# Kernel optimization log

Measured on AMD Instinct MI355X. Metric: run time of the kernel, lower is better.

## Reference

```python
import jax, jax.numpy as jnp
import numpy as np

B = 4; E_PER = 100_000; E = B * E_PER
N_NODES = 50_000; N_REL = 500; D = 64; D_LG = 256
K_PER_VI = 20; S_VI = E // K_PER_VI          # 20000 sorted vi segments
S_VJ_PER = 5_000; S_VJ = B * S_VJ_PER        # 20000 unsorted vj segments
N_MEM = 131_072
INTERACT = ((0, 3), (0, 2, 3), (0, 4), (0, 2, 4), (1, 3), (1, 2, 3), (1, 4), (1, 2, 4))


def _build_edges():
    rng = np.random.default_rng(0)
    idx_vi = np.repeat(np.arange(S_VI), K_PER_VI)          # sorted segment ids
    gpb = S_VI // B
    eg = idx_vi // gpb                                     # sorted by eg_idx too
    vi = rng.integers(0, N_NODES, S_VI)[idx_vi]
    idx_vj = np.empty(E, dtype=np.int64)
    for b in range(B):
        loc = np.concatenate([np.arange(S_VJ_PER), rng.integers(0, S_VJ_PER, E_PER - S_VJ_PER)])
        rng.shuffle(loc)
        idx_vj[b * E_PER:(b + 1) * E_PER] = b * S_VJ_PER + loc  # every group non-empty
    vj = rng.integers(0, N_NODES, S_VJ)[idx_vj]            # consistent (eg, vj) per group
    rel = rng.integers(0, N_REL, E)
    e2vi = rng.integers(0, N_MEM, E)
    e2vj = rng.integers(0, N_MEM, E)
    return np.stack([eg, vi, vj, rel, idx_vi, idx_vj, e2vi, e2vj], axis=1).astype(np.int32)


def setup_inputs() -> dict:
    key = jax.random.key(0)
    ks = jax.random.split(key, 10)
    return {
        "node_attention": jax.random.uniform(ks[0], (B, N_NODES), jnp.float32),
        "scanned_edges": jnp.asarray(_build_edges()),
        "edges_y": jax.random.uniform(ks[1], (E,), jnp.float32),
        "hidden_uncon": jax.random.normal(ks[2], (1, N_NODES, D_LG), jnp.float32),
        "hidden_con": jax.random.normal(ks[3], (N_MEM, D), jnp.float32),
        "Wc": jax.random.normal(ks[4], (D, D), jnp.float32) / np.sqrt(D).astype(np.float32),
        "bc": jnp.zeros((D,), jnp.float32),
        "Wu": jax.random.normal(ks[5], (D_LG, D), jnp.float32) / np.sqrt(D_LG).astype(np.float32),
        "bu": jnp.zeros((D,), jnp.float32),
        "rel_table": jax.random.normal(ks[6], (N_REL, D), jnp.float32) * 0.05,
        "ws": jax.random.normal(ks[7], (len(INTERACT), D), jnp.float32) / np.sqrt(float(len(INTERACT))).astype(np.float32) if False else jax.random.normal(ks[7], (len(INTERACT), D), jnp.float32) * (1.0 / np.sqrt(len(INTERACT)).astype(np.float32)),
        "fb": jnp.zeros((D,), jnp.float32),
        "out_w": jax.random.normal(ks[8], (D,), jnp.float32),
        "out_b": jnp.zeros((D,), jnp.float32),
        "n_vi_segments": S_VI,
        "n_vj_segments": S_VJ,
    }


def reference(node_attention, scanned_edges, edges_y, hidden_uncon, hidden_con,
              Wc, bc, Wu, bu, rel_table, ws, fb, out_w, out_b,
              n_vi_segments, n_vj_segments):
    eg, vi, vj, rel = (scanned_edges[:, i] for i in range(4))
    idx_vi, idx_vj, e2vi, e2vj = (scanned_edges[:, i] for i in range(4, 8))
    # projections (proj_con / proj_uncon, tanh Dense)
    hc = jnp.tanh(hidden_con @ Wc + bc)          # [N_MEM, D]
    hu = jnp.tanh(hidden_uncon @ Wu + bu)[0]     # [n_nodes, D]; batch_size==1 path of Node2Edge
    # Node2Edge gathers
    feats = (hc[e2vi], hu[vi], rel_table[rel], hc[e2vj], hu[vj])  # each [E, D]
    # F layer: weighted sum of elementwise interaction products
    out = fb
    for k, idxs in enumerate(INTERACT):
        x = feats[idxs[0]]
        for i in idxs[1:]:
            x = x * feats[i]
        out = out + x * ws[k]
    out = jax.nn.relu(out) * out_w + out_b
    logits = jnp.sum(out, axis=1)                # [E]
    # NeighborSoftmax at 'vi' (sorted segment softmax)
    m = jax.ops.segment_max(logits, idx_vi, num_segments=n_vi_segments)
    ex = jnp.exp(logits - m[idx_vi])
    den = jax.ops.segment_sum(ex, idx_vi, num_segments=n_vi_segments)
    transition = ex / den[idx_vi]
    # attention flow: gather source attention, weight, aggregate at vj
    trans_att = transition * node_attention[eg, vi] * edges_y
    aggr = jax.ops.segment_sum(trans_att, idx_vj, num_segments=n_vj_segments)
    b_g = jax.ops.segment_max(eg, idx_vj, num_segments=n_vj_segments)
    vj_g = jax.ops.segment_max(vj, idx_vj, num_segments=n_vj_segments)
    new_node_attention = jnp.zeros_like(node_attention).at[b_g, vj_g].add(aggr)
    return new_node_attention
```

## Files before the change

### kernel.cpp

```cpp
#include <hip/hip_runtime.h>
#include <hip/hip_bf16.h>
#include <hip/hip_fp16.h>

#define D 64
#define KPER 20

typedef __attribute__((ext_vector_type(8))) short short8;
typedef __attribute__((ext_vector_type(4))) float floatx4;

__device__ __forceinline__ unsigned short f2bfu(float x) {
    __hip_bfloat16 h = __float2bfloat16(x);
    return *reinterpret_cast<unsigned short*>(&h);
}
__device__ __forceinline__ unsigned short f2hu(float x) {
    __half h = __float2half(x);
    return *reinterpret_cast<unsigned short*>(&h);
}
union UH2 { unsigned u; __half2 h; };
__device__ __forceinline__ __half2 u2h2(unsigned u) { UH2 x; x.u = u; return x.h; }

__device__ __forceinline__ __half2 pk_max(__half2 a, __half2 b) {
    __half2 r;
    asm("v_pk_max_f16 %0, %1, %2" : "=v"(r) : "v"(a), "v"(b));
    return r;
}

__device__ __forceinline__ float fast_tanh(float x) {
    float xc = fminf(fmaxf(x, -15.f), 15.f);
    float e = __expf(2.f * xc);
    return 1.f - 2.f * __builtin_amdgcn_rcpf(1.f + e);
}

template<int CTRL>
__device__ __forceinline__ float dpp_add(float x) {
    int t = __builtin_amdgcn_update_dpp(0, __float_as_int(x), CTRL, 0xf, 0xf, true);
    return x + __int_as_float(t);
}
template<int CTRL>
__device__ __forceinline__ float dpp_max(float x) {
    int xi = __float_as_int(x);
    int t = __builtin_amdgcn_update_dpp(xi, xi, CTRL, 0xf, 0xf, false);
    return fmaxf(x, __int_as_float(t));
}
__device__ __forceinline__ float wave_sum_b(float x) {
    x = dpp_add<0x111>(x); x = dpp_add<0x112>(x);
    x = dpp_add<0x114>(x); x = dpp_add<0x118>(x);
    x = dpp_add<0x142>(x); x = dpp_add<0x143>(x);
    return __int_as_float(__builtin_amdgcn_readlane(__float_as_int(x), 63));
}
__device__ __forceinline__ float wave_max_b(float x) {
    x = dpp_max<0x111>(x); x = dpp_max<0x112>(x);
    x = dpp_max<0x114>(x); x = dpp_max<0x118>(x);
    x = dpp_max<0x142>(x); x = dpp_max<0x143>(x);
    return __int_as_float(__builtin_amdgcn_readlane(__float_as_int(x), 63));
}
__device__ __forceinline__ float row16_sum(float x) {
    x = dpp_add<0x111>(x); x = dpp_add<0x112>(x);
    x = dpp_add<0x114>(x); x = dpp_add<0x118>(x);
    return x;
}

__global__ __launch_bounds__(256) void prep(
        const float* __restrict__ Wc, const float* __restrict__ Wu,
        const float* __restrict__ relf, const float* __restrict__ wsf,
        const float* __restrict__ fbf,
        unsigned short* __restrict__ Wcp, unsigned short* __restrict__ Wup,
        unsigned short* __restrict__ relb, unsigned short* __restrict__ wsh,
        unsigned short* __restrict__ fbh, float* __restrict__ outz,
        int nout, int nrel) {
    int tid = blockIdx.x * 256 + threadIdx.x;
    int nth = gridDim.x * 256;
    for (int i = tid; i < 4 * 2 * 64 * 8; i += nth) {
        int j = i & 7, lane = (i >> 3) & 63, f = i >> 9;
        int ct = f >> 1, kt = f & 1;
        int m = lane & 15, quad = lane >> 4;
        Wcp[i] = f2bfu(Wc[(kt * 32 + quad * 8 + j) * 64 + ct * 16 + m]);
    }
    for (int i = tid; i < 4 * 8 * 64 * 8; i += nth) {
        int j = i & 7, lane = (i >> 3) & 63, f = i >> 9;
        int ct = f >> 3, kt = f & 7;
        int m = lane & 15, quad = lane >> 4;
        Wup[i] = f2bfu(Wu[(kt * 32 + quad * 8 + j) * 64 + ct * 16 + m]);
    }
    for (int i = tid; i < nrel; i += nth) relb[i] = f2hu(relf[i]);
    for (int i = tid; i < 8 * D; i += nth) wsh[i] = f2hu(wsf[i]);
    for (int i = tid; i < D; i += nth) fbh[i] = f2hu(fbf[i]);
    for (int i = tid; i < nout; i += nth) outz[i] = 0.0f;
}

__device__ __forceinline__ void proj64_pair(const float* __restrict__ h,
        const unsigned short* __restrict__ Wp, const float* __restrict__ b,
        unsigned short* __restrict__ out, int rt0) {
    constexpr int K = 64, KT = 2, CTN = 4;
    int lane = threadIdx.x & 63;
    int m = lane & 15, quad = lane >> 4;
    short8 bfr[CTN][KT];
    #pragma unroll
    for (int ct = 0; ct < CTN; ++ct)
        #pragma unroll
        for (int kt = 0; kt < KT; ++kt)
            bfr[ct][kt] = *(const short8*)(Wp + (((ct * 2 + kt) * 64 + lane) << 3));
    float bv[CTN];
    #pragma unroll
    for (int ct = 0; ct < CTN; ++ct) bv[ct] = b[ct * 16 + m];
    int rt1 = rt0 + 1;
    const float* hrow0 = h + (size_t)(rt0 * 16 + m) * K + quad * 8;
    const float* hrow1 = h + (size_t)(rt1 * 16 + m) * K + quad * 8;
    floatx4 a0[KT][2], a1[KT][2];
    #pragma unroll
    for (int kt = 0; kt < KT; ++kt) {
        a0[kt][0] = *(const floatx4*)(hrow0 + kt * 32);
        a0[kt][1] = *(const floatx4*)(hrow0 + kt * 32 + 4);
        a1[kt][0] = *(const floatx4*)(hrow1 + kt * 32);
        a1[kt][1] = *(const floatx4*)(hrow1 + kt * 32 + 4);
    }
    #pragma unroll
    for (int t = 0; t < 2; ++t) {
        floatx4 (*ar)[2] = t ? a1 : a0;
        int rt = t ? rt1 : rt0;
        floatx4 acc[CTN];
        #pragma unroll
        for (int ct = 0; ct < CTN; ++ct) acc[ct] = floatx4{0.f, 0.f, 0.f, 0.f};
        #pragma unroll
        for (int kt = 0; kt < KT; ++kt) {
            short8 af;
            #pragma unroll
            for (int j = 0; j < 4; ++j) {
                af[j]     = (short)f2bfu(ar[kt][0][j]);
                af[j + 4] = (short)f2bfu(ar[kt][1][j]);
            }
            #pragma unroll
            for (int ct = 0; ct < CTN; ++ct)
                acc[ct] = __builtin_amdgcn_mfma_f32_16x16x32_bf16(af, bfr[ct][kt], acc[ct], 0, 0, 0);
        }
        #pragma unroll
        for (int ct = 0; ct < CTN; ++ct) {
            int col = ct * 16 + m;
            #pragma unroll
            for (int reg = 0; reg < 4; ++reg) {
                int row = rt * 16 + quad * 4 + reg;
                out[(size_t)row * 64 + col] = f2hu(fast_tanh(acc[ct][reg] + bv[ct]));
            }
        }
    }
}

__device__ __forceinline__ void proj256_body(const float* __restrict__ h,
        const unsigned short* __restrict__ Wp, const float* __restrict__ b,
        unsigned short* __restrict__ out, int ct0, int rt0, int rtstride, int ntiles) {
    constexpr int K = 256, KT = 8, CTN = 2;
    int lane = threadIdx.x & 63;
    int m = lane & 15, quad = lane >> 4;
    short8 bfr[CTN][KT];
    #pragma unroll
    for (int ct = 0; ct < CTN; ++ct)
        #pragma unroll
        for (int kt = 0; kt < KT; ++kt)
            bfr[ct][kt] = *(const short8*)(Wp + ((((ct0 + ct) * 8 + kt) * 64 + lane) << 3));
    float bv[CTN];
    #pragma unroll
    for (int ct = 0; ct < CTN; ++ct) bv[ct] = b[(ct0 + ct) * 16 + m];
    for (int rt = rt0; rt < ntiles; rt += rtstride) {
        floatx4 acc[CTN];
        #pragma unroll
        for (int ct = 0; ct < CTN; ++ct) acc[ct] = floatx4{0.f, 0.f, 0.f, 0.f};
        const float* hrow = h + (size_t)(rt * 16 + m) * K + quad * 8;
        #pragma unroll
        for (int kt = 0; kt < KT; ++kt) {
            floatx4 v0 = *(const floatx4*)(hrow + kt * 32);
            floatx4 v1 = *(const floatx4*)(hrow + kt * 32 + 4);
            short8 af;
            #pragma unroll
            for (int j = 0; j < 4; ++j) {
                af[j]     = (short)f2bfu(v0[j]);
                af[j + 4] = (short)f2bfu(v1[j]);
            }
            #pragma unroll
            for (int ct = 0; ct < CTN; ++ct)
                acc[ct] = __builtin_amdgcn_mfma_f32_16x16x32_bf16(af, bfr[ct][kt], acc[ct], 0, 0, 0);
        }
        #pragma unroll
        for (int ct = 0; ct < CTN; ++ct) {
            int col = (ct0 + ct) * 16 + m;
            #pragma unroll
            for (int reg = 0; reg < 4; ++reg) {
                int row = rt * 16 + quad * 4 + reg;
                out[(size_t)row * 64 + col] = f2hu(fast_tanh(acc[ct][reg] + bv[ct]));
            }
        }
    }
}

__global__ __launch_bounds__(256) void proj_fused(
        const float* __restrict__ hcon, const unsigned short* __restrict__ Wcp,
        const float* __restrict__ bc,
        const float* __restrict__ hun, const unsigned short* __restrict__ Wup,
        const float* __restrict__ bu,
        unsigned short* __restrict__ hc, unsigned short* __restrict__ hu,
        int t64, int t256, int g64, int g256) {
    int bid = blockIdx.x;
    int w = threadIdx.x >> 6;
    if (bid < g256) {
        int wid = bid * 4 + w;
        int half = wid & 1;
        proj256_body(hun, Wup, bu, hu, half * 2, wid >> 1, g256 * 2, t256);
    } else {
        int wid = (bid - g256) * 4 + w;
        proj64_pair(hcon, Wcp, bc, hc, wid * 2);
    }
}

__device__ __forceinline__ float seg_myl(
        const uint2* __restrict__ G0, const uint2* __restrict__ G2,
        const uint2* __restrict__ G3, const uint2* __restrict__ G4,
        uint2 F1u, const uint2* __restrict__ wku, uint2 fbu, floatx4 owv,
        int lane, int l2, __half2 z2) {
    __half2 f1[2]  = { u2h2(F1u.x), u2h2(F1u.y) };
    __half2 fb2[2] = { u2h2(fbu.x), u2h2(fbu.y) };
    float myl = -INFINITY;
    #pragma unroll
    for (int i = 0; i < 5; ++i) {
        float acc = 0.f;
        #pragma unroll
        for (int p = 0; p < 2; ++p) {
            __half2 F0 = u2h2(p ? G0[i].y : G0[i].x);
            __half2 F2 = u2h2(p ? G2[i].y : G2[i].x);
            __half2 F3 = u2h2(p ? G3[i].y : G3[i].x);
            __half2 F4 = u2h2(p ? G4[i].y : G4[i].x);
            __half2 w0 = u2h2(p ? wku[0].y : wku[0].x);
            __half2 w1 = u2h2(p ? wku[1].y : wku[1].x);
            __half2 w2 = u2h2(p ? wku[2].y : wku[2].x);
            __half2 w3 = u2h2(p ? wku[3].y : wku[3].x);
            __half2 w4 = u2h2(p ? wku[4].y : wku[4].x);
            __half2 w5 = u2h2(p ? wku[5].y : wku[5].x);
            __half2 w6 = u2h2(p ? wku[6].y : wku[6].x);
            __half2 w7 = u2h2(p ? wku[7].y : wku[7].x);
            __half2 t1 = __hfma2(F2, w1, w0);
            __half2 t2 = __hfma2(F2, w5, w4);
            __half2 t3 = __hfma2(F2, w3, w2);
            __half2 t4 = __hfma2(F2, w7, w6);
            __half2 uu = __hfma2(F0, t1, __hmul2(f1[p], t2));
            __half2 vv = __hfma2(F0, t3, __hmul2(f1[p], t4));
            __half2 od = __hfma2(F3, uu, __hfma2(F4, vv, fb2[p]));
            __half2 r  = pk_max(od, z2);
            float2 rf  = __half22float2(r);
            acc = fmaf(rf.x, owv[2 * p], fmaf(rf.y, owv[2 * p + 1], acc));
        }
        float rs = row16_sum(acc);
        float tot = __shfl(rs, ((lane & 3) << 4) + 15);
        myl = (l2 == i) ? tot : myl;
    }
    return myl;
}

__global__ __launch_bounds__(256) void edge_kernel(
        const float* __restrict__ natt, const int* __restrict__ edges,
        const float* __restrict__ ey, const unsigned short* __restrict__ hc,
        const unsigned short* __restrict__ hu, const unsigned short* __restrict__ relt,
        const unsigned short* __restrict__ wsh, const unsigned short* __restrict__ fbh,
        const float* __restrict__ outw, float* __restrict__ out, int N) {
    int lane = threadIdx.x & 63;
    int g = lane >> 4, sub = lane & 15;
    int l2 = lane >> 2;
    int wid = blockIdx.x * 4 + (threadIdx.x >> 6);
    long baseA = (long)(wid * 2) * KPER;
    long baseB = baseA + KPER;
    const int* ebA = edges + baseA * 8;
    const int* ebB = edges + baseB * 8;

    int2 h0A = *(const int2*)ebA;
    int2 h0B = *(const int2*)ebB;
    const int* egpA = ebA + g * 8;
    const int* egpB = ebB + g * 8;
    int2 m23A[5], m67A[5], m23B[5], m67B[5];
    #pragma unroll
    for (int i = 0; i < 5; ++i) {
        m23A[i] = *(const int2*)(egpA + i * 32 + 2);
        m67A[i] = *(const int2*)(egpA + i * 32 + 6);
        m23B[i] = *(const int2*)(egpB + i * 32 + 2);
        m67B[i] = *(const int2*)(egpB + i * 32 + 6);
    }
    int myvjA = 0, myvjB = 0; float eyA = 0.f, eyB = 0.f;
    if (lane < KPER) {
        myvjA = ebA[lane * 8 + 2];
        myvjB = ebB[lane * 8 + 2];
        eyA = ey[baseA + lane];
        eyB = ey[baseB + lane];
    }
    int egA = __builtin_amdgcn_readfirstlane(h0A.x);
    int viA = __builtin_amdgcn_readfirstlane(h0A.y);
    int egB = __builtin_amdgcn_readfirstlane(h0B.x);
    int viB = __builtin_amdgcn_readfirstlane(h0B.y);

    uint2 GA0[5], GA2[5], GA3[5], GA4[5];
    #pragma unroll
    for (int i = 0; i < 5; ++i) {
        GA0[i] = *(const uint2*)(hc   + (size_t)m67A[i].x * D + sub * 4);
        GA2[i] = *(const uint2*)(relt + (size_t)m23A[i].y * D + sub * 4);
        GA3[i] = *(const uint2*)(hc   + (size_t)m67A[i].y * D + sub * 4);
        GA4[i] = *(const uint2*)(hu   + (size_t)m23A[i].x * D + sub * 4);
    }
    uint2 F1A = *(const uint2*)(hu + (size_t)viA * D + sub * 4);
    uint2 GB0[5], GB2[5], GB3[5], GB4[5];
    #pragma unroll
    for (int i = 0; i < 5; ++i) {
        GB0[i] = *(const uint2*)(hc   + (size_t)m67B[i].x * D + sub * 4);
        GB2[i] = *(const uint2*)(relt + (size_t)m23B[i].y * D + sub * 4);
        GB3[i] = *(const uint2*)(hc   + (size_t)m67B[i].y * D + sub * 4);
        GB4[i] = *(const uint2*)(hu   + (size_t)m23B[i].x * D + sub * 4);
    }
    uint2 F1B = *(const uint2*)(hu + (size_t)viB * D + sub * 4);
    float naA = natt[(size_t)egA * N + viA];
    float naB = natt[(size_t)egB * N + viB];

    uint2 wku[8];
    #pragma unroll
    for (int k = 0; k < 8; ++k) wku[k] = *(const uint2*)(wsh + k * D + sub * 4);
    uint2 fbu = *(const uint2*)(fbh + sub * 4);
    floatx4 owv = *(const floatx4*)(outw + sub * 4);
    __half2 z2 = __float2half2_rn(0.f);

    float mylA = seg_myl(GA0, GA2, GA3, GA4, F1A, wku, fbu, owv, lane, l2, z2);
    float mxA = wave_max_b(mylA);
    float exA = __expf(mylA - mxA);
    float denA = wave_sum_b(exA);
    if (lane < KPER) {
        float t = (exA / denA) * naA * eyA;
        atomicAdd(out + (size_t)egA * N + myvjA, t);
    }
    float mylB = seg_myl(GB0, GB2, GB3, GB4, F1B, wku, fbu, owv, lane, l2, z2);
    float mxB = wave_max_b(mylB);
    float exB = __expf(mylB - mxB);
    float denB = wave_sum_b(exB);
    if (lane < KPER) {
        float t = (exB / denB) * naB * eyB;
        atomicAdd(out + (size_t)egB * N + myvjB, t);
    }
}

extern "C" void kernel_launch(void* const* d_in, const int* in_sizes, int n_in,
                              void* d_out, int out_size, void* d_ws, size_t ws_size,
                              hipStream_t stream) {
    const float* natt = (const float*)d_in[0];
    const int*   edges = (const int*)d_in[1];
    const float* ey   = (const float*)d_in[2];
    const float* hun  = (const float*)d_in[3];
    const float* hcon = (const float*)d_in[4];
    const float* Wc   = (const float*)d_in[5];
    const float* bc   = (const float*)d_in[6];
    const float* Wu   = (const float*)d_in[7];
    const float* bu   = (const float*)d_in[8];
    const float* relt = (const float*)d_in[9];
    const float* wsm  = (const float*)d_in[10];
    const float* fb   = (const float*)d_in[11];
    const float* outw = (const float*)d_in[12];
    float* out = (float*)d_out;

    int E    = in_sizes[2];
    int S    = E / KPER;
    int nmem = in_sizes[4] / D;
    int N    = in_sizes[3] / 256;
    int nrel = in_sizes[9];

    int t64  = nmem / 16;
    int t256 = N / 16;
    int g64  = t64 / 8;
    int g256 = 800;

    unsigned short* hc  = (unsigned short*)d_ws;
    unsigned short* hu  = hc + (size_t)nmem * D;
    unsigned short* rb  = hu + (size_t)N * D;
    unsigned short* Wcp = rb + nrel;
    unsigned short* Wup = Wcp + 4096;
    unsigned short* wsh = Wup + 16384;
    unsigned short* fbh = wsh + 8 * D;

    prep<<<64, 256, 0, stream>>>(Wc, Wu, relt, wsm, fb, Wcp, Wup, rb, wsh, fbh,
                                 out, out_size, nrel);
    proj_fused<<<g256 + g64, 256, 0, stream>>>(hcon, Wcp, bc, hun, Wup, bu,
                                               hc, hu, t64, t256, g64, g256);
    edge_kernel<<<S / 8, 256, 0, stream>>>(natt, edges, ey, hc, hu, rb,
                                           wsh, fbh, outw, out, N);
}
```

Baseline: 198.1 us.

## Split edge kernel into logits kernel and segment softmax-scatter kernel

Replaces the fused per-segment edge kernel, which had each wave hold two full 20-edge segments of gathered features in registers, with two kernels. The first computes per-edge logits with 16 lanes per edge in a simple loop and writes them to a workspace buffer. The second does the segment softmax and atomic scatter per segment. This is meant to cut register pressure and raise occupancy for the gather-heavy part. The cost is an extra launch plus a write and re-read of the logits array.

Result: slower. 225.7 us (+14.0%).

```diff
diff --git a/kernel.cpp b/kernel.cpp
--- a/kernel.cpp
+++ b/kernel.cpp
@@ -210,108 +210,48 @@
     }
 }
 
-__device__ __forceinline__ float seg_myl(
-        const uint2* __restrict__ G0, const uint2* __restrict__ G2,
-        const uint2* __restrict__ G3, const uint2* __restrict__ G4,
-        uint2 F1u, const uint2* __restrict__ wku, uint2 fbu, floatx4 owv,
-        int lane, int l2, __half2 z2) {
-    __half2 f1[2]  = { u2h2(F1u.x), u2h2(F1u.y) };
-    __half2 fb2[2] = { u2h2(fbu.x), u2h2(fbu.y) };
-    float myl = -INFINITY;
-    #pragma unroll
-    for (int i = 0; i < 5; ++i) {
-        float acc = 0.f;
-        #pragma unroll
-        for (int p = 0; p < 2; ++p) {
-            __half2 F0 = u2h2(p ? G0[i].y : G0[i].x);
-            __half2 F2 = u2h2(p ? G2[i].y : G2[i].x);
-            __half2 F3 = u2h2(p ? G3[i].y : G3[i].x);
-            __half2 F4 = u2h2(p ? G4[i].y : G4[i].x);
-            __half2 w0 = u2h2(p ? wku[0].y : wku[0].x);
-            __half2 w1 = u2h2(p ? wku[1].y : wku[1].x);
-            __half2 w2 = u2h2(p ? wku[2].y : wku[2].x);
-            __half2 w3 = u2h2(p ? wku[3].y : wku[3].x);
-            __half2 w4 = u2h2(p ? wku[4].y : wku[4].x);
-            __half2 w5 = u2h2(p ? wku[5].y : wku[5].x);
-            __half2 w6 = u2h2(p ? wku[6].y : wku[6].x);
-            __half2 w7 = u2h2(p ? wku[7].y : wku[7].x);
-            __half2 t1 = __hfma2(F2, w1, w0);
-            __half2 t2 = __hfma2(F2, w5, w4);
-            __half2 t3 = __hfma2(F2, w3, w2);
-            __half2 t4 = __hfma2(F2, w7, w6);
-            __half2 uu = __hfma2(F0, t1, __hmul2(f1[p], t2));
-            __half2 vv = __hfma2(F0, t3, __hmul2(f1[p], t4));
-            __half2 od = __hfma2(F3, uu, __hfma2(F4, vv, fb2[p]));
-            __half2 r  = pk_max(od, z2);
-            float2 rf  = __half22float2(r);
-            acc = fmaf(rf.x, owv[2 * p], fmaf(rf.y, owv[2 * p + 1], acc));
-        }
-        float rs = row16_sum(acc);
-        float tot = __shfl(rs, ((lane & 3) << 4) + 15);
-        myl = (l2 == i) ? tot : myl;
-    }
-    return myl;
-}
-
-__global__ __launch_bounds__(256) void edge_kernel(
-        const float* __restrict__ natt, const int* __restrict__ edges,
-        const float* __restrict__ ey, const unsigned short* __restrict__ hc,
+__device__ __forceinline__ float edge_acc(
+        uint2 G0, uint2 G2, uint2 G3, uint2 G4, uint2 F1u,
+        const uint2* __restrict__ wku, uint2 fbu, floatx4 owv, __half2 z2) {
+    float acc = 0.f;
+    #pragma unroll
+    for (int p = 0; p < 2; ++p) {
+        __half2 F0 = u2h2(p ? G0.y : G0.x);
+        __half2 F2 = u2h2(p ? G2.y : G2.x);
+        __half2 F3 = u2h2(p ? G3.y : G3.x);
+        __half2 F4 = u2h2(p ? G4.y : G4.x);
+        __half2 f1 = u2h2(p ? F1u.y : F1u.x);
+        __half2 fb2 = u2h2(p ? fbu.y : fbu.x);
+        __half2 w0 = u2h2(p ? wku[0].y : wku[0].x);
+        __half2 w1 = u2h2(p ? wku[1].y : wku[1].x);
+        __half2 w2 = u2h2(p ? wku[2].y : wku[2].x);
+        __half2 w3 = u2h2(p ? wku[3].y : wku[3].x);
+        __half2 w4 = u2h2(p ? wku[4].y : wku[4].x);
+        __half2 w5 = u2h2(p ? wku[5].y : wku[5].x);
+        __half2 w6 = u2h2(p ? wku[6].y : wku[6].x);
+        __half2 w7 = u2h2(p ? wku[7].y : wku[7].x);
+        __half2 t1 = __hfma2(F2, w1, w0);
+        __half2 t2 = __hfma2(F2, w5, w4);
+        __half2 t3 = __hfma2(F2, w3, w2);
+        __half2 t4 = __hfma2(F2, w7, w6);
+        __half2 uu = __hfma2(F0, t1, __hmul2(f1, t2));
+        __half2 vv = __hfma2(F0, t3, __hmul2(f1, t4));
+        __half2 od = __hfma2(F3, uu, __hfma2(F4, vv, fb2));
+        __half2 r  = pk_max(od, z2);
+        float2 rf  = __half22float2(r);
+        acc = fmaf(rf.x, owv[2 * p], fmaf(rf.y, owv[2 * p + 1], acc));
+    }
+    return acc;
+}
+
+__global__ __launch_bounds__(256) void logits_kernel(
+        const int* __restrict__ edges, const unsigned short* __restrict__ hc,
         const unsigned short* __restrict__ hu, const unsigned short* __restrict__ relt,
         const unsigned short* __restrict__ wsh, const unsigned short* __restrict__ fbh,
-        const float* __restrict__ outw, float* __restrict__ out, int N) {
-    int lane = threadIdx.x & 63;
-    int g = lane >> 4, sub = lane & 15;
-    int l2 = lane >> 2;
-    int wid = blockIdx.x * 4 + (threadIdx.x >> 6);
-    long baseA = (long)(wid * 2) * KPER;
-    long baseB = baseA + KPER;
-    const int* ebA = edges + baseA * 8;
-    const int* ebB = edges + baseB * 8;
-
-    int2 h0A = *(const int2*)ebA;
-    int2 h0B = *(const int2*)ebB;
-    const int* egpA = ebA + g * 8;
-    const int* egpB = ebB + g * 8;
-    int2 m23A[5], m67A[5], m23B[5], m67B[5];
-    #pragma unroll
-    for (int i = 0; i < 5; ++i) {
-        m23A[i] = *(const int2*)(egpA + i * 32 + 2);
-        m67A[i] = *(const int2*)(egpA + i * 32 + 6);
-        m23B[i] = *(const int2*)(egpB + i * 32 + 2);
-        m67B[i] = *(const int2*)(egpB + i * 32 + 6);
-    }
-    int myvjA = 0, myvjB = 0; float eyA = 0.f, eyB = 0.f;
-    if (lane < KPER) {
-        myvjA = ebA[lane * 8 + 2];
-        myvjB = ebB[lane * 8 + 2];
-        eyA = ey[baseA + lane];
-        eyB = ey[baseB + lane];
-    }
-    int egA = __builtin_amdgcn_readfirstlane(h0A.x);
-    int viA = __builtin_amdgcn_readfirstlane(h0A.y);
-    int egB = __builtin_amdgcn_readfirstlane(h0B.x);
-    int viB = __builtin_amdgcn_readfirstlane(h0B.y);
-
-    uint2 GA0[5], GA2[5], GA3[5], GA4[5];
-    #pragma unroll
-    for (int i = 0; i < 5; ++i) {
-        GA0[i] = *(const uint2*)(hc   + (size_t)m67A[i].x * D + sub * 4);
-        GA2[i] = *(const uint2*)(relt + (size_t)m23A[i].y * D + sub * 4);
-        GA3[i] = *(const uint2*)(hc   + (size_t)m67A[i].y * D + sub * 4);
-        GA4[i] = *(const uint2*)(hu   + (size_t)m23A[i].x * D + sub * 4);
-    }
-    uint2 F1A = *(const uint2*)(hu + (size_t)viA * D + sub * 4);
-    uint2 GB0[5], GB2[5], GB3[5], GB4[5];
-    #pragma unroll
-    for (int i = 0; i < 5; ++i) {
-        GB0[i] = *(const uint2*)(hc   + (size_t)m67B[i].x * D + sub * 4);
-        GB2[i] = *(const uint2*)(relt + (size_t)m23B[i].y * D + sub * 4);
-        GB3[i] = *(const uint2*)(hc   + (size_t)m67B[i].y * D + sub * 4);
-        GB4[i] = *(const uint2*)(hu   + (size_t)m23B[i].x * D + sub * 4);
-    }
-    uint2 F1B = *(const uint2*)(hu + (size_t)viB * D + sub * 4);
-    float naA = natt[(size_t)egA * N + viA];
-    float naB = natt[(size_t)egB * N + viB];
+        const float* __restrict__ outw, float* __restrict__ logits, int E) {
+    int sub = threadIdx.x & 15;
+    int sg  = threadIdx.x >> 4;
+    int e0  = blockIdx.x * 128 + sg;
 
     uint2 wku[8];
     #pragma unroll
@@ -320,21 +260,46 @@
     floatx4 owv = *(const floatx4*)(outw + sub * 4);
     __half2 z2 = __float2half2_rn(0.f);
 
-    float mylA = seg_myl(GA0, GA2, GA3, GA4, F1A, wku, fbu, owv, lane, l2, z2);
-    float mxA = wave_max_b(mylA);
-    float exA = __expf(mylA - mxA);
-    float denA = wave_sum_b(exA);
+    #pragma unroll 2
+    for (int k = 0; k < 8; ++k) {
+        int e = e0 + k * 16;
+        const int* eb = edges + (size_t)e * 8;
+        int4 m0 = *(const int4*)eb;
+        int2 m6 = *(const int2*)(eb + 6);
+        uint2 G0 = *(const uint2*)(hc   + (size_t)m6.x * D + sub * 4);
+        uint2 G2 = *(const uint2*)(relt + (size_t)m0.w * D + sub * 4);
+        uint2 G3 = *(const uint2*)(hc   + (size_t)m6.y * D + sub * 4);
+        uint2 G4 = *(const uint2*)(hu   + (size_t)m0.z * D + sub * 4);
+        uint2 F1 = *(const uint2*)(hu   + (size_t)m0.y * D + sub * 4);
+        float acc = edge_acc(G0, G2, G3, G4, F1, wku, fbu, owv, z2);
+        float rs = row16_sum(acc);
+        if (sub == 15) logits[e] = rs;
+    }
+}
+
+__global__ __launch_bounds__(256) void softmax_scatter(
+        const float* __restrict__ natt, const int* __restrict__ edges,
+        const float* __restrict__ ey, const float* __restrict__ logits,
+        float* __restrict__ out, int N) {
+    int lane = threadIdx.x & 63;
+    int s = blockIdx.x * 4 + (threadIdx.x >> 6);
+    long base = (long)s * KPER;
+    const int* eb = edges + base * 8;
+    int eg = __builtin_amdgcn_readfirstlane(eb[0]);
+    int vi = __builtin_amdgcn_readfirstlane(eb[1]);
+    float myl = -INFINITY; int myvj = 0; float eyv = 0.f;
     if (lane < KPER) {
-        float t = (exA / denA) * naA * eyA;
-        atomicAdd(out + (size_t)egA * N + myvjA, t);
-    }
-    float mylB = seg_myl(GB0, GB2, GB3, GB4, F1B, wku, fbu, owv, lane, l2, z2);
-    float mxB = wave_max_b(mylB);
-    float exB = __expf(mylB - mxB);
-    float denB = wave_sum_b(exB);
+        myl  = logits[base + lane];
+        myvj = eb[lane * 8 + 2];
+        eyv  = ey[base + lane];
+    }
+    float na = natt[(size_t)eg * N + vi];
+    float mx = wave_max_b(myl);
+    float ex = __expf(myl - mx);
+    float den = wave_sum_b(ex);
     if (lane < KPER) {
-        float t = (exB / denB) * naB * eyB;
-        atomicAdd(out + (size_t)egB * N + myvjB, t);
+        float t = (ex / den) * na * eyv;
+        atomicAdd(out + (size_t)eg * N + myvj, t);
     }
 }
 
@@ -374,11 +339,13 @@
     unsigned short* Wup = Wcp + 4096;
     unsigned short* wsh = Wup + 16384;
     unsigned short* fbh = wsh + 8 * D;
+    float* logits = (float*)(fbh + D);
 
     prep<<<64, 256, 0, stream>>>(Wc, Wu, relt, wsm, fb, Wcp, Wup, rb, wsh, fbh,
                                  out, out_size, nrel);
     proj_fused<<<g256 + g64, 256, 0, stream>>>(hcon, Wcp, bc, hun, Wup, bu,
                                                hc, hu, t64, t256, g64, g256);
-    edge_kernel<<<S / 8, 256, 0, stream>>>(natt, edges, ey, hc, hu, rb,
-                                           wsh, fbh, outw, out, N);
-}
+    logits_kernel<<<E / 128, 256, 0, stream>>>(edges, hc, hu, rb, wsh, fbh,
+                                               outw, logits, E);
+    softmax_scatter<<<S / 4, 256, 0, stream>>>(natt, edges, ey, logits, out, N);
+}
```

## Software-pipeline edge gathers one step ahead and use packed bf16 conversion

Applied to the files above, without the earlier changes.

Replaces the up-front batch of all per-edge gathers for both segments with a 10-step loop that prefetches the next step's four feature rows while computing the current one, with a scheduling barrier between them. This lowers register pressure and may raise occupancy. The cost is fewer loads in flight per wave, so more gather latency is exposed. The projection kernels also switch the float-to-bf16 packing to the v_cvt_pk_bf16_f32 instruction, converting two values per instruction.

Result: no change. 199.3 us (+0.6%).

```diff
diff --git a/kernel.cpp b/kernel.cpp
--- a/kernel.cpp
+++ b/kernel.cpp
@@ -18,6 +18,12 @@
 }
 union UH2 { unsigned u; __half2 h; };
 __device__ __forceinline__ __half2 u2h2(unsigned u) { UH2 x; x.u = u; return x.h; }
+
+__device__ __forceinline__ unsigned cvt2bf(float lo, float hi) {
+    unsigned r;
+    asm("v_cvt_pk_bf16_f32 %0, %1, %2" : "=v"(r) : "v"(lo), "v"(hi));
+    return r;
+}
 
 __device__ __forceinline__ __half2 pk_max(__half2 a, __half2 b) {
     __half2 r;
@@ -123,12 +129,12 @@
         for (int ct = 0; ct < CTN; ++ct) acc[ct] = floatx4{0.f, 0.f, 0.f, 0.f};
         #pragma unroll
         for (int kt = 0; kt < KT; ++kt) {
-            short8 af;
-            #pragma unroll
-            for (int j = 0; j < 4; ++j) {
-                af[j]     = (short)f2bfu(ar[kt][0][j]);
-                af[j + 4] = (short)f2bfu(ar[kt][1][j]);
-            }
+            union { uint4 u; short8 s; } cc;
+            cc.u.x = cvt2bf(ar[kt][0][0], ar[kt][0][1]);
+            cc.u.y = cvt2bf(ar[kt][0][2], ar[kt][0][3]);
+            cc.u.z = cvt2bf(ar[kt][1][0], ar[kt][1][1]);
+            cc.u.w = cvt2bf(ar[kt][1][2], ar[kt][1][3]);
+            short8 af = cc.s;
             #pragma unroll
             for (int ct = 0; ct < CTN; ++ct)
                 acc[ct] = __builtin_amdgcn_mfma_f32_16x16x32_bf16(af, bfr[ct][kt], acc[ct], 0, 0, 0);
@@ -169,12 +175,12 @@
         for (int kt = 0; kt < KT; ++kt) {
             floatx4 v0 = *(const floatx4*)(hrow + kt * 32);
             floatx4 v1 = *(const floatx4*)(hrow + kt * 32 + 4);
-            short8 af;
-            #pragma unroll
-            for (int j = 0; j < 4; ++j) {
-                af[j]     = (short)f2bfu(v0[j]);
-                af[j + 4] = (short)f2bfu(v1[j]);
-            }
+            union { uint4 u; short8 s; } cc;
+            cc.u.x = cvt2bf(v0[0], v0[1]);
+            cc.u.y = cvt2bf(v0[2], v0[3]);
+            cc.u.z = cvt2bf(v1[0], v1[1]);
+            cc.u.w = cvt2bf(v1[2], v1[3]);
+            short8 af = cc.s;
             #pragma unroll
             for (int ct = 0; ct < CTN; ++ct)
                 acc[ct] = __builtin_amdgcn_mfma_f32_16x16x32_bf16(af, bfr[ct][kt], acc[ct], 0, 0, 0);
@@ -210,47 +216,38 @@
     }
 }
 
-__device__ __forceinline__ float seg_myl(
-        const uint2* __restrict__ G0, const uint2* __restrict__ G2,
-        const uint2* __restrict__ G3, const uint2* __restrict__ G4,
-        uint2 F1u, const uint2* __restrict__ wku, uint2 fbu, floatx4 owv,
-        int lane, int l2, __half2 z2) {
-    __half2 f1[2]  = { u2h2(F1u.x), u2h2(F1u.y) };
-    __half2 fb2[2] = { u2h2(fbu.x), u2h2(fbu.y) };
-    float myl = -INFINITY;
-    #pragma unroll
-    for (int i = 0; i < 5; ++i) {
-        float acc = 0.f;
-        #pragma unroll
-        for (int p = 0; p < 2; ++p) {
-            __half2 F0 = u2h2(p ? G0[i].y : G0[i].x);
-            __half2 F2 = u2h2(p ? G2[i].y : G2[i].x);
-            __half2 F3 = u2h2(p ? G3[i].y : G3[i].x);
-            __half2 F4 = u2h2(p ? G4[i].y : G4[i].x);
-            __half2 w0 = u2h2(p ? wku[0].y : wku[0].x);
-            __half2 w1 = u2h2(p ? wku[1].y : wku[1].x);
-            __half2 w2 = u2h2(p ? wku[2].y : wku[2].x);
-            __half2 w3 = u2h2(p ? wku[3].y : wku[3].x);
-            __half2 w4 = u2h2(p ? wku[4].y : wku[4].x);
-            __half2 w5 = u2h2(p ? wku[5].y : wku[5].x);
-            __half2 w6 = u2h2(p ? wku[6].y : wku[6].x);
-            __half2 w7 = u2h2(p ? wku[7].y : wku[7].x);
-            __half2 t1 = __hfma2(F2, w1, w0);
-            __half2 t2 = __hfma2(F2, w5, w4);
-            __half2 t3 = __hfma2(F2, w3, w2);
-            __half2 t4 = __hfma2(F2, w7, w6);
-            __half2 uu = __hfma2(F0, t1, __hmul2(f1[p], t2));
-            __half2 vv = __hfma2(F0, t3, __hmul2(f1[p], t4));
-            __half2 od = __hfma2(F3, uu, __hfma2(F4, vv, fb2[p]));
-            __half2 r  = pk_max(od, z2);
-            float2 rf  = __half22float2(r);
-            acc = fmaf(rf.x, owv[2 * p], fmaf(rf.y, owv[2 * p + 1], acc));
-        }
-        float rs = row16_sum(acc);
-        float tot = __shfl(rs, ((lane & 3) << 4) + 15);
-        myl = (l2 == i) ? tot : myl;
-    }
-    return myl;
+__device__ __forceinline__ float edge_acc(
+        uint2 G0, uint2 G2, uint2 G3, uint2 G4, uint2 F1u,
+        const uint2* __restrict__ wku, uint2 fbu, floatx4 owv, __half2 z2) {
+    float acc = 0.f;
+    #pragma unroll
+    for (int p = 0; p < 2; ++p) {
+        __half2 F0 = u2h2(p ? G0.y : G0.x);
+        __half2 F2 = u2h2(p ? G2.y : G2.x);
+        __half2 F3 = u2h2(p ? G3.y : G3.x);
+        __half2 F4 = u2h2(p ? G4.y : G4.x);
+        __half2 f1 = u2h2(p ? F1u.y : F1u.x);
+        __half2 fb2 = u2h2(p ? fbu.y : fbu.x);
+        __half2 w0 = u2h2(p ? wku[0].y : wku[0].x);
+        __half2 w1 = u2h2(p ? wku[1].y : wku[1].x);
+        __half2 w2 = u2h2(p ? wku[2].y : wku[2].x);
+        __half2 w3 = u2h2(p ? wku[3].y : wku[3].x);
+        __half2 w4 = u2h2(p ? wku[4].y : wku[4].x);
+        __half2 w5 = u2h2(p ? wku[5].y : wku[5].x);
+        __half2 w6 = u2h2(p ? wku[6].y : wku[6].x);
+        __half2 w7 = u2h2(p ? wku[7].y : wku[7].x);
+        __half2 t1 = __hfma2(F2, w1, w0);
+        __half2 t2 = __hfma2(F2, w5, w4);
+        __half2 t3 = __hfma2(F2, w3, w2);
+        __half2 t4 = __hfma2(F2, w7, w6);
+        __half2 uu = __hfma2(F0, t1, __hmul2(f1, t2));
+        __half2 vv = __hfma2(F0, t3, __hmul2(f1, t4));
+        __half2 od = __hfma2(F3, uu, __hfma2(F4, vv, fb2));
+        __half2 r  = pk_max(od, z2);
+        float2 rf  = __half22float2(r);
+        acc = fmaf(rf.x, owv[2 * p], fmaf(rf.y, owv[2 * p + 1], acc));
+    }
+    return acc;
 }
 
 __global__ __launch_bounds__(256) void edge_kernel(
@@ -291,24 +288,7 @@
     int viA = __builtin_amdgcn_readfirstlane(h0A.y);
     int egB = __builtin_amdgcn_readfirstlane(h0B.x);
     int viB = __builtin_amdgcn_readfirstlane(h0B.y);
-
-    uint2 GA0[5], GA2[5], GA3[5], GA4[5];
-    #pragma unroll
-    for (int i = 0; i < 5; ++i) {
-        GA0[i] = *(const uint2*)(hc   + (size_t)m67A[i].x * D + sub * 4);
-        GA2[i] = *(const uint2*)(relt + (size_t)m23A[i].y * D + sub * 4);
-        GA3[i] = *(const uint2*)(hc   + (size_t)m67A[i].y * D + sub * 4);
-        GA4[i] = *(const uint2*)(hu   + (size_t)m23A[i].x * D + sub * 4);
-    }
     uint2 F1A = *(const uint2*)(hu + (size_t)viA * D + sub * 4);
-    uint2 GB0[5], GB2[5], GB3[5], GB4[5];
-    #pragma unroll
-    for (int i = 0; i < 5; ++i) {
-        GB0[i] = *(const uint2*)(hc   + (size_t)m67B[i].x * D + sub * 4);
-        GB2[i] = *(const uint2*)(relt + (size_t)m23B[i].y * D + sub * 4);
-        GB3[i] = *(const uint2*)(hc   + (size_t)m67B[i].y * D + sub * 4);
-        GB4[i] = *(const uint2*)(hu   + (size_t)m23B[i].x * D + sub * 4);
-    }
     uint2 F1B = *(const uint2*)(hu + (size_t)viB * D + sub * 4);
     float naA = natt[(size_t)egA * N + viA];
     float naB = natt[(size_t)egB * N + viB];
@@ -320,7 +300,34 @@
     floatx4 owv = *(const floatx4*)(outw + sub * 4);
     __half2 z2 = __float2half2_rn(0.f);
 
-    float mylA = seg_myl(GA0, GA2, GA3, GA4, F1A, wku, fbu, owv, lane, l2, z2);
+    float mylA = -INFINITY, mylB = -INFINITY;
+    uint2 c0 = *(const uint2*)(hc   + (size_t)m67A[0].x * D + sub * 4);
+    uint2 c2 = *(const uint2*)(relt + (size_t)m23A[0].y * D + sub * 4);
+    uint2 c3 = *(const uint2*)(hc   + (size_t)m67A[0].y * D + sub * 4);
+    uint2 c4 = *(const uint2*)(hu   + (size_t)m23A[0].x * D + sub * 4);
+    #pragma unroll
+    for (int t = 0; t < 10; ++t) {
+        uint2 n0 = c0, n2 = c2, n3 = c3, n4 = c4;
+        if (t < 9) {
+            const int tn = t + 1;
+            const int2* p23 = (tn < 5) ? m23A : m23B;
+            const int2* p67 = (tn < 5) ? m67A : m67B;
+            const int ii = (tn < 5) ? tn : tn - 5;
+            n0 = *(const uint2*)(hc   + (size_t)p67[ii].x * D + sub * 4);
+            n2 = *(const uint2*)(relt + (size_t)p23[ii].y * D + sub * 4);
+            n3 = *(const uint2*)(hc   + (size_t)p67[ii].y * D + sub * 4);
+            n4 = *(const uint2*)(hu   + (size_t)p23[ii].x * D + sub * 4);
+        }
+        __builtin_amdgcn_sched_barrier(0);
+        uint2 F1 = (t < 5) ? F1A : F1B;
+        float acc = edge_acc(c0, c2, c3, c4, F1, wku, fbu, owv, z2);
+        float rs = row16_sum(acc);
+        float tot = __shfl(rs, ((lane & 3) << 4) + 15);
+        if (t < 5) mylA = (l2 == t) ? tot : mylA;
+        else       mylB = (l2 == (t - 5)) ? tot : mylB;
+        c0 = n0; c2 = n2; c3 = n3; c4 = n4;
+    }
+
     float mxA = wave_max_b(mylA);
     float exA = __expf(mylA - mxA);
     float denA = wave_sum_b(exA);
@@ -328,7 +335,6 @@
         float t = (exA / denA) * naA * eyA;
         atomicAdd(out + (size_t)egA * N + myvjA, t);
     }
-    float mylB = seg_myl(GB0, GB2, GB3, GB4, F1B, wku, fbu, owv, lane, l2, z2);
     float mxB = wave_max_b(mylB);
     float exB = __expf(mylB - mxB);
     float denB = wave_sum_b(exB);
```
